# Performance work log

Measured on AMD Instinct MI355X. Metric: run time of the kernel, lower is better.

## Reference

```python
import jax, jax.numpy as jnp
import numpy as np

H, W = 224, 224  # image_size


def setup_inputs() -> dict:
    key = jax.random.key(0)
    k1, k2, k3, k4 = jax.random.split(key, 4)
    B, N = 16, 500000
    # unit-scale object point cloud
    vertices = jax.random.normal(k1, (B, N, 3), dtype=jnp.float32) * 0.5
    # proper rotation matrices via QR of random gaussians
    A = jax.random.normal(k2, (B, 3, 3), dtype=jnp.float32)
    rotation, _ = jnp.linalg.qr(A)
    # camera looks down +z; object placed ~3 units in front
    tz = jax.random.uniform(k3, (B, 1), minval=2.5, maxval=3.5, dtype=jnp.float32)
    txy = jax.random.normal(k4, (B, 2), dtype=jnp.float32) * 0.1
    translation = jnp.concatenate([txy, tz], axis=1)
    K = jnp.array([[250.0, 0.0, 112.0],
                   [0.0, 250.0, 112.0],
                   [0.0, 0.0, 1.0]], dtype=jnp.float32)
    camera_intrinsics = jnp.broadcast_to(K, (B, 3, 3))
    return {
        "vertices": vertices,
        "rotation": rotation,
        "translation": translation,
        "camera_intrinsics": camera_intrinsics,
    }


def reference(vertices, rotation, translation, camera_intrinsics):
    B, N, _ = vertices.shape
    # world -> camera: bmm(vertices, R^T) + t
    vc = jnp.einsum('bnj,bkj->bnk', vertices, rotation) + translation[:, None, :]
    fx = camera_intrinsics[:, 0, 0][:, None]
    fy = camera_intrinsics[:, 1, 1][:, None]
    cx = camera_intrinsics[:, 0, 2][:, None]
    cy = camera_intrinsics[:, 1, 2][:, None]
    Z = vc[:, :, 2] + 1e-8
    u = fx * (vc[:, :, 0] / Z) + cx          # (B, N)
    v = fy * (vc[:, :, 1] / Z) + cy
    # Python int() truncates toward zero -> jnp.trunc
    ui = jnp.trunc(u).astype(jnp.int32)
    vi = jnp.trunc(v).astype(jnp.int32)
    depths = vc[:, :, 2]                     # (B, N) values written to buffer
    valid = (ui >= 0) & (ui < W) & (vi >= 0) & (vi < H)
    P = B * H * W
    b_idx = jnp.arange(B, dtype=jnp.int32)[:, None]
    pix = jnp.where(valid, b_idx * (H * W) + vi * W + ui, P).ravel()  # OOB -> dump segment
    # winner of each pixel is the point with the largest flattened index.
    order = jnp.arange(B * N, dtype=jnp.int32)
    win = jax.ops.segment_max(order, pix, num_segments=P + 1)[:P]
    has = win >= 0  # empty segments are filled with int32 min (negative)
    buf = jnp.where(has, depths.ravel()[jnp.clip(win, 0)], jnp.float32(0.0))
    return buf.reshape(B, 1, H, W)
```

## Files before the change

kernel.cpp:

```cpp
#include <hip/hip_runtime.h>
#include <stdint.h>

#define RH 224
#define RW 224
#define HW (RH * RW)
#define NCHUNK 16
#define BLOCK_THREADS 1024
#define LDSW (HW / 2)


#pragma clang fp contract(off)

__device__ __forceinline__ float dot3_fwd_nofma(float v0, float v1, float v2,
                                                float R0, float R1, float R2,
                                                float t) {
#pragma clang fp contract(off)
    const float p0 = v0 * R0;
    const float p1 = v1 * R1;
    const float p2 = v2 * R2;
    float acc = p0 + p1;
    acc = acc + p2;
    acc = acc + t;
    return acc;
}

__global__ __launch_bounds__(BLOCK_THREADS) void
proj16_kernel(const float* __restrict__ vertices,
              const float* __restrict__ rotation,
              const float* __restrict__ translation,
              const float* __restrict__ Kmat,
              unsigned int* __restrict__ ws,
              int N, int chunk) {
#pragma clang fp contract(off)
    extern __shared__ unsigned int sbuf[];

    const int blk = (int)blockIdx.x;
    const int c   = blk % NCHUNK;
    const int b   = blk / NCHUNK;

    {
        uint4* s4 = (uint4*)sbuf;
        const uint4 z = {0u, 0u, 0u, 0u};
        for (int j = threadIdx.x; j < LDSW / 4; j += BLOCK_THREADS) s4[j] = z;
    }
    __syncthreads();

    const float* R = rotation + b * 9;
    const float* t = translation + b * 3;
    const float* k = Kmat + b * 9;
    const float fx = k[0], cx = k[2], fy = k[4], cy = k[5];
    const float R00 = R[0], R01 = R[1], R02 = R[2];
    const float R10 = R[3], R11 = R[4], R12 = R[5];
    const float R20 = R[6], R21 = R[7], R22 = R[8];
    const float t0 = t[0], t1 = t[1], t2 = t[2];

    const int n_beg  = c * chunk;
    const int n_end  = min(N, n_beg + chunk);
    const int nquads = (n_end - n_beg + 3) >> 2;

    for (int q = threadIdx.x; q < nquads; q += BLOCK_THREADS) {
        const int n0 = n_beg + (q << 2);
        const float4* vp = (const float4*)(vertices + ((size_t)b * N + n0) * 3);
        const float4 f0 = vp[0], f1 = vp[1], f2 = vp[2];
        const float pxv[4][3] = {{f0.x, f0.y, f0.z}, {f0.w, f1.x, f1.y},
                                 {f1.z, f1.w, f2.x}, {f2.y, f2.z, f2.w}};
#pragma unroll
        for (int kk = 0; kk < 4; ++kk) {
            const int n = n0 + kk;
            if (n >= n_end) break;
            const float v0 = pxv[kk][0], v1 = pxv[kk][1], v2 = pxv[kk][2];

            const float y = dot3_fwd_nofma(v0, v1, v2, R10, R11, R12, t1);
            const float z = dot3_fwd_nofma(v0, v1, v2, R20, R21, R22, t2);
            const float Z = z + 1e-8f;
            const float qy = y / Z;
            float w = fy * qy;
            w = w + cy;
            const float tv = truncf(w);
            if (!(tv >= 0.0f && tv < (float)RH)) continue;

            const float x = dot3_fwd_nofma(v0, v1, v2, R00, R01, R02, t0);
            const float qx = x / Z;
            float u = fx * qx;
            u = u + cx;
            const float tu = truncf(u);
            if (!(tu >= 0.0f && tu < (float)RW)) continue;

            const unsigned int p  = (unsigned int)((int)tv * RW + (int)tu);
            const unsigned int sh = (p & 1u) << 4;
            const unsigned int val = (unsigned int)(n - n_beg + 1);
            unsigned int* wp = &sbuf[p >> 1];
            unsigned int cur = *wp;
            while (((cur >> sh) & 0xFFFFu) < val) {
                const unsigned int nw =
                    (cur & ~(0xFFFFu << sh)) | (val << sh);
                const unsigned int prev = atomicCAS(wp, cur, nw);
                if (prev == cur) break;
                cur = prev;
            }
        }
    }
    __syncthreads();

    uint4* dst = (uint4*)(ws + (size_t)blk * LDSW);
    const uint4* src = (const uint4*)sbuf;
    for (int j = threadIdx.x; j < LDSW / 4; j += BLOCK_THREADS)
        dst[j] = src[j];
}

__global__ void resolve16_kernel(const unsigned short* __restrict__ ws16,
                                 const float* __restrict__ vertices,
                                 const float* __restrict__ rotation,
                                 const float* __restrict__ translation,
                                 float* __restrict__ out, int N, int chunk,
                                 int P) {
#pragma clang fp contract(off)
    const int g = blockIdx.x * blockDim.x + threadIdx.x;
    if (g >= P / 4) return;
    const int i0  = g << 2;
    const int b   = i0 / HW;
    const int pix = i0 - b * HW;

    const unsigned short* base = ws16 + ((size_t)b * NCHUNK) * HW + pix;
    unsigned int m0 = 0u, m1 = 0u, m2 = 0u, m3 = 0u;
#pragma unroll
    for (int c = 0; c < NCHUNK; ++c) {
        const uint2 v2 = *(const uint2*)(base + (size_t)c * HW);
        const unsigned int ck = (unsigned int)(c + 1) << 16;
        unsigned int v;
        v = v2.x & 0xFFFFu; if (v) m0 = ck | v;
        v = v2.x >> 16;     if (v) m1 = ck | v;
        v = v2.y & 0xFFFFu; if (v) m2 = ck | v;
        v = v2.y >> 16;     if (v) m3 = ck | v;
    }

    const unsigned int mm[4] = {m0, m1, m2, m3};
    float4 o;
    float* op = (float*)&o;
#pragma unroll
    for (int j = 0; j < 4; ++j) {
        float depth = 0.0f;
        const unsigned int m = mm[j];
        if (m != 0u) {
            const int c = (int)(m >> 16) - 1;
            const int n = c * chunk + (int)(m & 0xFFFFu) - 1;
            const float* v = vertices + ((size_t)b * (size_t)N + (size_t)n) * 3;
            const float* R = rotation + b * 9;
            depth = dot3_fwd_nofma(v[0], v[1], v[2], R[6], R[7], R[8],
                                   translation[b * 3 + 2]);
        }
        op[j] = depth;
    }
    *(float4*)(out + i0) = o;
}

#define NSTRIPE 2
#define STRIPE_ROWS (RH / NSTRIPE)
#define STRIPE_PX (STRIPE_ROWS * RW)

__global__ __launch_bounds__(BLOCK_THREADS) void
proj_fb_kernel(const float* __restrict__ vertices,
               const float* __restrict__ rotation,
               const float* __restrict__ translation,
               const float* __restrict__ Kmat,
               unsigned int* __restrict__ win, int N) {
#pragma clang fp contract(off)
    extern __shared__ unsigned int sbuf[];
    const int blk = (int)blockIdx.x;
    const int s   = blk & (NSTRIPE - 1);
    const int c   = (blk >> 1) & 7;
    const int b   = blk >> 4;
    for (int j = threadIdx.x; j < STRIPE_PX; j += BLOCK_THREADS) sbuf[j] = 0u;
    __syncthreads();
    const float* R = rotation + b * 9;
    const float* t = translation + b * 3;
    const float* k = Kmat + b * 9;
    const float fx = k[0], cx = k[2], fy = k[4], cy = k[5];
    const float R00 = R[0], R01 = R[1], R02 = R[2];
    const float R10 = R[3], R11 = R[4], R12 = R[5];
    const float R20 = R[6], R21 = R[7], R22 = R[8];
    const float t0 = t[0], t1 = t[1], t2 = t[2];
    const int chunk  = (N + 7) / 8;
    const int n_beg  = c * chunk;
    const int n_end  = min(N, n_beg + chunk);
    const int nquads = (n_end - n_beg + 3) >> 2;
    const float v_lo = (float)(s * STRIPE_ROWS);
    const float v_hi = (float)((s + 1) * STRIPE_ROWS);
    for (int q = threadIdx.x; q < nquads; q += BLOCK_THREADS) {
        const int n0 = n_beg + (q << 2);
        const float4* vp = (const float4*)(vertices + ((size_t)b * N + n0) * 3);
        const float4 f0 = vp[0], f1 = vp[1], f2 = vp[2];
        const float pxv[4][3] = {{f0.x, f0.y, f0.z}, {f0.w, f1.x, f1.y},
                                 {f1.z, f1.w, f2.x}, {f2.y, f2.z, f2.w}};
#pragma unroll
        for (int kk = 0; kk < 4; ++kk) {
            const int n = n0 + kk;
            if (n >= n_end) break;
            const float v0 = pxv[kk][0], v1 = pxv[kk][1], v2 = pxv[kk][2];
            const float y = dot3_fwd_nofma(v0, v1, v2, R10, R11, R12, t1);
            const float z = dot3_fwd_nofma(v0, v1, v2, R20, R21, R22, t2);
            const float Z = z + 1e-8f;
            const float qy = y / Z;
            float w = fy * qy;
            w = w + cy;
            const float tv = truncf(w);
            if (!(tv >= v_lo && tv < v_hi)) continue;
            const float x = dot3_fwd_nofma(v0, v1, v2, R00, R01, R02, t0);
            const float qx = x / Z;
            float u = fx * qx;
            u = u + cx;
            const float tu = truncf(u);
            if (!(tu >= 0.0f && tu < (float)RW)) continue;
            const int slot = ((int)tv - s * STRIPE_ROWS) * RW + (int)tu;
            atomicMax(&sbuf[slot], (unsigned int)(b * N + n) + 1u);
        }
    }
    __syncthreads();
    unsigned int* g = win + b * HW + s * STRIPE_PX;
    for (int j = threadIdx.x; j < STRIPE_PX; j += BLOCK_THREADS) {
        const unsigned int val = sbuf[j];
        if (val) atomicMax(&g[j], val);
    }
}

__global__ void resolve_fb_kernel(unsigned int* __restrict__ buf,
                                  const float* __restrict__ vertices,
                                  const float* __restrict__ rotation,
                                  const float* __restrict__ translation,
                                  int N, int P) {
#pragma clang fp contract(off)
    const int i = blockIdx.x * blockDim.x + threadIdx.x;
    if (i >= P) return;
    const unsigned int o1 = buf[i];
    float depth = 0.0f;
    if (o1 != 0u) {
        const unsigned int o = o1 - 1u;
        const int b = (int)(o / (unsigned int)N);
        const int n = (int)(o % (unsigned int)N);
        const float* v = vertices + ((size_t)b * (size_t)N + (size_t)n) * 3;
        const float* R = rotation + b * 9;
        depth = dot3_fwd_nofma(v[0], v[1], v[2], R[6], R[7], R[8],
                               translation[b * 3 + 2]);
    }
    buf[i] = __float_as_uint(depth);
}

extern "C" void kernel_launch(void* const* d_in, const int* in_sizes, int n_in,
                              void* d_out, int out_size, void* d_ws, size_t ws_size,
                              hipStream_t stream) {
    const float* vertices    = (const float*)d_in[0];
    const float* rotation    = (const float*)d_in[1];
    const float* translation = (const float*)d_in[2];
    const float* Kmat        = (const float*)d_in[3];

    const int B = in_sizes[1] / 9;
    const int N = in_sizes[0] / (3 * B);
    const int P = B * HW;
    const int nblocks = B * NCHUNK;
    const int chunk = (((N + NCHUNK - 1) / NCHUNK) + 3) & ~3;

    const size_t ws_needed = (size_t)nblocks * LDSW * sizeof(unsigned int);

    if (ws_size >= ws_needed && chunk < 65536 && (P & 3) == 0) {
        unsigned int* ws = (unsigned int*)d_ws;
        proj16_kernel<<<nblocks, BLOCK_THREADS,
                        LDSW * sizeof(unsigned int), stream>>>(
            vertices, rotation, translation, Kmat, ws, N, chunk);
        const int rthreads = P / 4;
        const int rblocks = (rthreads + 255) / 256;
        resolve16_kernel<<<rblocks, 256, 0, stream>>>(
            (const unsigned short*)d_ws, vertices, rotation, translation,
            (float*)d_out, N, chunk, P);
    } else {
        unsigned int* win = (unsigned int*)d_out;
        hipMemsetAsync(win, 0, (size_t)P * sizeof(unsigned int), stream);
        proj_fb_kernel<<<B * 16, BLOCK_THREADS,
                         STRIPE_PX * sizeof(unsigned int), stream>>>(
            vertices, rotation, translation, Kmat, win, N);
        const int rblocks = (P + 255) / 256;
        resolve_fb_kernel<<<rblocks, 256, 0, stream>>>(win, vertices, rotation,
                                                       translation, N, P);
    }
}
```

Measured before the change: 47.42 us.

## Overlap LDS zeroing with projection by buffering pixel codes in registers

The projection kernel now computes up to 32 pixel indices per thread into registers before the barrier, so vertex loads and projection arithmetic overlap with zeroing the shared-memory z-buffer. The atomicCAS scatter runs after the barrier, and the kernel adds a launch-bounds occupancy hint. The register-staged scheme only works when a chunk fits in 8 quads per thread, so the fast path is now guarded by that check. This raises register pressure in exchange for removing the serial zero-then-compute dependency.

```diff
diff --git a/kernel.cpp b/kernel.cpp
--- a/kernel.cpp
+++ b/kernel.cpp
@@ -24,7 +24,7 @@
     return acc;
 }
 
-__global__ __launch_bounds__(BLOCK_THREADS) void
+__global__ __launch_bounds__(BLOCK_THREADS, 4) void
 proj16_kernel(const float* __restrict__ vertices,
               const float* __restrict__ rotation,
               const float* __restrict__ translation,
@@ -37,13 +37,13 @@
     const int blk = (int)blockIdx.x;
     const int c   = blk % NCHUNK;
     const int b   = blk / NCHUNK;
+    const int tid = (int)threadIdx.x;
 
     {
         uint4* s4 = (uint4*)sbuf;
         const uint4 z = {0u, 0u, 0u, 0u};
-        for (int j = threadIdx.x; j < LDSW / 4; j += BLOCK_THREADS) s4[j] = z;
-    }
-    __syncthreads();
+        for (int j = tid; j < LDSW / 4; j += BLOCK_THREADS) s4[j] = z;
+    }
 
     const float* R = rotation + b * 9;
     const float* t = translation + b * 3;
@@ -54,46 +54,76 @@
     const float R20 = R[6], R21 = R[7], R22 = R[8];
     const float t0 = t[0], t1 = t[1], t2 = t[2];
 
-    const int n_beg  = c * chunk;
-    const int n_end  = min(N, n_beg + chunk);
-    const int nquads = (n_end - n_beg + 3) >> 2;
-
-    for (int q = threadIdx.x; q < nquads; q += BLOCK_THREADS) {
-        const int n0 = n_beg + (q << 2);
-        const float4* vp = (const float4*)(vertices + ((size_t)b * N + n0) * 3);
-        const float4 f0 = vp[0], f1 = vp[1], f2 = vp[2];
-        const float pxv[4][3] = {{f0.x, f0.y, f0.z}, {f0.w, f1.x, f1.y},
-                                 {f1.z, f1.w, f2.x}, {f2.y, f2.z, f2.w}};
-#pragma unroll
-        for (int kk = 0; kk < 4; ++kk) {
-            const int n = n0 + kk;
-            if (n >= n_end) break;
-            const float v0 = pxv[kk][0], v1 = pxv[kk][1], v2 = pxv[kk][2];
-
-            const float y = dot3_fwd_nofma(v0, v1, v2, R10, R11, R12, t1);
-            const float z = dot3_fwd_nofma(v0, v1, v2, R20, R21, R22, t2);
-            const float Z = z + 1e-8f;
-            const float qy = y / Z;
-            float w = fy * qy;
-            w = w + cy;
-            const float tv = truncf(w);
-            if (!(tv >= 0.0f && tv < (float)RH)) continue;
-
-            const float x = dot3_fwd_nofma(v0, v1, v2, R00, R01, R02, t0);
-            const float qx = x / Z;
-            float u = fx * qx;
-            u = u + cx;
-            const float tu = truncf(u);
-            if (!(tu >= 0.0f && tu < (float)RW)) continue;
-
-            const unsigned int p  = (unsigned int)((int)tv * RW + (int)tu);
-            const unsigned int sh = (p & 1u) << 4;
-            const unsigned int val = (unsigned int)(n - n_beg + 1);
+    const int n_beg   = c * chunk;
+    const int n_end   = min(N, n_beg + chunk);
+    const int nquads  = (n_end - n_beg + 3) >> 2;
+
+    unsigned int pix[16];
+#pragma unroll
+    for (int j = 0; j < 8; ++j) {
+        unsigned int lo = 0xFFFFu | (0xFFFFu << 16);
+        unsigned int hi = 0xFFFFu | (0xFFFFu << 16);
+        const int q = j * BLOCK_THREADS + tid;
+        if (q < nquads) {
+            const int n0 = n_beg + (q << 2);
+            const float4* vp =
+                (const float4*)(vertices + ((size_t)b * N + n0) * 3);
+            const float4 f0 = vp[0], f1 = vp[1], f2 = vp[2];
+            const float pxv[4][3] = {{f0.x, f0.y, f0.z}, {f0.w, f1.x, f1.y},
+                                     {f1.z, f1.w, f2.x}, {f2.y, f2.z, f2.w}};
+            unsigned int code[4];
+#pragma unroll
+            for (int kk = 0; kk < 4; ++kk) {
+                code[kk] = 0xFFFFu;
+                const int n = n0 + kk;
+                if (n >= n_end) continue;
+                const float v0 = pxv[kk][0], v1 = pxv[kk][1], v2 = pxv[kk][2];
+
+                const float y = dot3_fwd_nofma(v0, v1, v2, R10, R11, R12, t1);
+                const float z = dot3_fwd_nofma(v0, v1, v2, R20, R21, R22, t2);
+                const float Z = z + 1e-8f;
+                const float qy = y / Z;
+                float w = fy * qy;
+                w = w + cy;
+                const float tv = truncf(w);
+                if (!(tv >= 0.0f && tv < (float)RH)) continue;
+
+                const float x = dot3_fwd_nofma(v0, v1, v2, R00, R01, R02, t0);
+                const float qx = x / Z;
+                float u = fx * qx;
+                u = u + cx;
+                const float tu = truncf(u);
+                if (!(tu >= 0.0f && tu < (float)RW)) continue;
+
+                code[kk] = (unsigned int)((int)tv * RW + (int)tu);
+            }
+            lo = code[0] | (code[1] << 16);
+            hi = code[2] | (code[3] << 16);
+        }
+        pix[2 * j + 0] = lo;
+        pix[2 * j + 1] = hi;
+    }
+
+    __syncthreads();
+
+#pragma unroll
+    for (int m = 0; m < 16; ++m) {
+        const int j  = m >> 1;
+        const int kb = (m & 1) << 1;
+        const unsigned int pk = pix[m];
+        const unsigned int vbase =
+            (unsigned int)(j * (BLOCK_THREADS * 4) + tid * 4) + 1u;
+#pragma unroll
+        for (int h = 0; h < 2; ++h) {
+            const unsigned int p = (h == 0) ? (pk & 0xFFFFu) : (pk >> 16);
+            if (p == 0xFFFFu) continue;
+            const unsigned int sh  = (p & 1u) << 4;
+            const unsigned int msk = 0xFFFFu << sh;
+            const unsigned int val = vbase + (unsigned int)(kb + h);
             unsigned int* wp = &sbuf[p >> 1];
             unsigned int cur = *wp;
             while (((cur >> sh) & 0xFFFFu) < val) {
-                const unsigned int nw =
-                    (cur & ~(0xFFFFu << sh)) | (val << sh);
+                const unsigned int nw = (cur & ~msk) | (val << sh);
                 const unsigned int prev = atomicCAS(wp, cur, nw);
                 if (prev == cur) break;
                 cur = prev;
@@ -104,7 +134,7 @@
 
     uint4* dst = (uint4*)(ws + (size_t)blk * LDSW);
     const uint4* src = (const uint4*)sbuf;
-    for (int j = threadIdx.x; j < LDSW / 4; j += BLOCK_THREADS)
+    for (int j = tid; j < LDSW / 4; j += BLOCK_THREADS)
         dst[j] = src[j];
 }
 
@@ -124,9 +154,9 @@
     const unsigned short* base = ws16 + ((size_t)b * NCHUNK) * HW + pix;
     unsigned int m0 = 0u, m1 = 0u, m2 = 0u, m3 = 0u;
 #pragma unroll
-    for (int c = 0; c < NCHUNK; ++c) {
-        const uint2 v2 = *(const uint2*)(base + (size_t)c * HW);
-        const unsigned int ck = (unsigned int)(c + 1) << 16;
+    for (int cc = 0; cc < NCHUNK; ++cc) {
+        const uint2 v2 = *(const uint2*)(base + (size_t)cc * HW);
+        const unsigned int ck = (unsigned int)(cc + 1) << 16;
         unsigned int v;
         v = v2.x & 0xFFFFu; if (v) m0 = ck | v;
         v = v2.x >> 16;     if (v) m1 = ck | v;
@@ -142,8 +172,8 @@
         float depth = 0.0f;
         const unsigned int m = mm[j];
         if (m != 0u) {
-            const int c = (int)(m >> 16) - 1;
-            const int n = c * chunk + (int)(m & 0xFFFFu) - 1;
+            const int cc = (int)(m >> 16) - 1;
+            const int n  = cc * chunk + (int)(m & 0xFFFFu) - 1;
             const float* v = vertices + ((size_t)b * (size_t)N + (size_t)n) * 3;
             const float* R = rotation + b * 9;
             depth = dot3_fwd_nofma(v[0], v[1], v[2], R[6], R[7], R[8],
@@ -260,8 +290,9 @@
     const int chunk = (((N + NCHUNK - 1) / NCHUNK) + 3) & ~3;
 
     const size_t ws_needed = (size_t)nblocks * LDSW * sizeof(unsigned int);
-
-    if (ws_size >= ws_needed && chunk < 65536 && (P & 3) == 0) {
+    const bool fits8 = ((chunk + 3) >> 2) <= 8 * BLOCK_THREADS;
+
+    if (ws_size >= ws_needed && chunk < 65536 && (P & 3) == 0 && fits8) {
         unsigned int* ws = (unsigned int*)d_ws;
         proj16_kernel<<<nblocks, BLOCK_THREADS,
                         LDSW * sizeof(unsigned int), stream>>>(
```

Result: slower. 50.80 us (+7.1%).
